# Optimization experiments

Hardware: AMD Instinct MI355X
Metric: run time of the kernel (lower is better)

The kernel has to match this reference:

```python
import jax, jax.numpy as jnp
import numpy as np

N = 1536           # candidates (== pre_nms_k, so pre-selection branch is identity)
H = W = 224        # mask resolution
NCLS = 80
SIGMA = 0.5
POST_NMS_K = 768
SCORE_THRESHOLD = 0.5
EPS = 1e-6


def setup_inputs() -> dict:
    key = jax.random.key(0)
    k1, k2, k3, k4, k5 = jax.random.split(key, 5)
    binary_masks = (jax.random.uniform(k1, (N, H, W)) > 0.5).astype(jnp.float32)
    seg_preds = jax.random.uniform(k2, (N, H, W), dtype=jnp.float32)
    scores = jax.random.uniform(k3, (N,), dtype=jnp.float32)
    cls_labels = jax.random.randint(k4, (N,), 0, NCLS, dtype=jnp.int32)
    cls_factors = jax.random.normal(k5, (N,), dtype=jnp.float32)
    mask_sum = binary_masks.reshape(N, -1).sum(axis=1)  # per-instance area
    return {
        "cls_labels": cls_labels,
        "scores": scores,
        "cls_factors": cls_factors,
        "seg_preds": seg_preds,
        "binary_masks": binary_masks,
        "mask_sum": mask_sum,
    }


def reference(cls_labels, scores, cls_factors, seg_preds, binary_masks, mask_sum):
    """Matrix NMS (SOLOv2) over binary masks; faithful to the torch source.

    Returns fixed-shape, zero-padded (seg_preds, scores, cls_labels, cls_factors)
    with POST_NMS_K rows; padding rows have score 0 / label -1.
    """
    n = scores.shape[0]  # == pre_nms_k, so the torch top-k pre-filter is a no-op
    flat = binary_masks.reshape(n, -1)                    # [N, H*W]
    intersection = flat @ flat.T                          # [N, N] pairwise overlap
    # NOTE: faithful to source: mask_sum.view(1,-1) + mask_sum.view(1,-1)
    # (i.e. 2 * area_j broadcast over rows), reproducing the original's math.
    mask_sum_tile = mask_sum[None, :] + mask_sum[None, :]
    union = mask_sum_tile - intersection
    iou = intersection / (union + EPS)
    iou = jnp.triu(iou, 1)
    labels_match = jnp.triu(
        (cls_labels[None, :] == cls_labels[:, None]).astype(iou.dtype), 1)
    decay_iou = iou * labels_match                        # [N, N]
    compensate_iou = decay_iou.max(axis=0)                # [N]
    comp_mat = compensate_iou[:, None]                    # expand(N,N).T of source
    # gaussian mode
    decay_coefficient = jnp.exp(-(decay_iou ** 2 - comp_mat ** 2) / SIGMA).min(axis=0)
    decayed_scores = scores * decay_coefficient
    valid = decayed_scores >= SCORE_THRESHOLD
    # torch code keeps ORIGINAL scores of surviving rows, then takes top post_nms_k
    sort_key = jnp.where(valid, scores, -1.0)
    _, idx = jax.lax.top_k(sort_key, POST_NMS_K)
    kept_valid = valid[idx]
    out_scores = jnp.where(kept_valid, scores[idx], 0.0)
    out_seg = jnp.where(kept_valid[:, None, None], seg_preds[idx], 0.0)
    out_labels = jnp.where(kept_valid, cls_labels[idx], -1)
    out_factors = jnp.where(kept_valid, cls_factors[idx], 0.0)
    return out_seg, out_scores, out_labels, out_factors
```

## Files before the change

kernel.cpp:

```cpp
#include <hip/hip_runtime.h>
#include <stdint.h>

typedef unsigned long long u64;
typedef unsigned int u32;
typedef unsigned short u16;

#define N_MASKS 1536
#define HW 50176
#define WORDS 784
#define NCLS 80
#define POST_NMS_K 768
#define SEG_ELEMS ((size_t)POST_NMS_K * HW)
#define KEYPAD 2048
#define BITS_BYTES ((size_t)N_MASKS * WORDS * 8)

#define MMAX 96
#define MAXPAIRS (MMAX*(MMAX-1)/2)
#define TW 112
#define TWP 113
#define NTILES (WORDS/TW)

__global__ __launch_bounds__(256) void pack_kernel(const float4* __restrict__ masks,
                                                   u64* __restrict__ bits) {
    int gid = blockIdx.x * blockDim.x + threadIdx.x;
    int wave = gid >> 6;
    int lane = gid & 63;
    float4 v = masks[(size_t)wave * 64 + lane];
    u64 b0 = __ballot(v.x > 0.5f);
    u64 b1 = __ballot(v.y > 0.5f);
    u64 b2 = __ballot(v.z > 0.5f);
    u64 b3 = __ballot(v.w > 0.5f);
    if (lane < 4) {
        u64 w = (lane == 0) ? b0 : (lane == 1) ? b1 : (lane == 2) ? b2 : b3;
        bits[(size_t)wave * 4 + lane] = w;
    }
}

__global__ __launch_bounds__(256) void classnms_kernel(
        const int* __restrict__ labels, const float* __restrict__ scores,
        const float* __restrict__ msum, const u64* __restrict__ bits,
        float* __restrict__ keys) {
    const int cls = blockIdx.x;
    const int tid = threadIdx.x;
    __shared__ int mem[MMAX];
    __shared__ float Sm[MMAX], Sc[MMAX];
    __shared__ u32 compS[MMAX], Ms[MMAX];
    __shared__ u16 lutAB[MAXPAIRS];
    __shared__ u32 Ipair[MAXPAIRS];
    __shared__ u64 rows[MMAX * TWP];
    __shared__ int scan[256];
    __shared__ int mtot;

    const int PER = N_MASKS / 256;
    int lab[PER]; int cnt = 0;
#pragma unroll
    for (int k = 0; k < PER; ++k) { lab[k] = labels[tid * PER + k]; cnt += (lab[k] == cls); }
    scan[tid] = cnt;
    __syncthreads();
    for (int off = 1; off < 256; off <<= 1) {
        int v = scan[tid];
        int u = (tid >= off) ? scan[tid - off] : 0;
        __syncthreads();
        scan[tid] = v + u;
        __syncthreads();
    }
    {
        int o = scan[tid] - cnt;
#pragma unroll
        for (int k = 0; k < PER; ++k)
            if (lab[k] == cls) mem[o++] = tid * PER + k;
    }
    if (tid == 255) mtot = scan[255];
    __syncthreads();
    const int m = mtot;
    const int np = m * (m - 1) / 2;

    for (int b = tid; b < m; b += 256) {
        int g = mem[b];
        Sm[b] = msum[g]; Sc[b] = scores[g];
        compS[b] = 0u; Ms[b] = 0u;
    }
    for (int p = tid; p < np; p += 256) {
        int bb = (int)((1.0 + sqrt(1.0 + 8.0 * (double)p)) * 0.5);
        while (bb * (bb - 1) / 2 > p) --bb;
        while ((bb + 1) * bb / 2 <= p) ++bb;
        int aa = p - bb * (bb - 1) / 2;
        lutAB[p] = (u16)((aa << 8) | bb);
        Ipair[p] = 0u;
    }

    for (int t = 0; t < NTILES; ++t) {
        __syncthreads();
        for (int idx = tid; idx < m * TW; idx += 256) {
            int r = idx / TW, w = idx - r * TW;
            rows[r * TWP + w] = bits[(size_t)mem[r] * WORDS + t * TW + w];
        }
        __syncthreads();
        for (int p = tid; p < np; p += 256) {
            int ab = lutAB[p];
            const u64* ra = &rows[(ab >> 8) * TWP];
            const u64* rb = &rows[(ab & 255) * TWP];
            u32 s = 0;
#pragma unroll 8
            for (int w = 0; w < TW; ++w) s += (u32)__popcll(ra[w] & rb[w]);
            Ipair[p] += s;
        }
    }
    __syncthreads();

    for (int p = tid; p < np; p += 256) {
        int ab = lutAB[p]; int bcol = ab & 255;
        float fI = (float)Ipair[p];
        float D = fI / (2.0f * Sm[bcol] - fI + 1e-6f);
        Ipair[p] = __float_as_uint(D);
        atomicMax(&compS[bcol], __float_as_uint(D));
    }
    __syncthreads();
    for (int p = tid; p < np; p += 256) {
        int ab = lutAB[p]; int aa = ab >> 8; int bcol = ab & 255;
        float D = __uint_as_float(Ipair[p]);
        float ca = __uint_as_float(compS[aa]);
        float v = fmaxf(D * D - ca * ca, 0.0f);
        atomicMax(&Ms[bcol], __float_as_uint(v));
    }
    __syncthreads();
    for (int b = tid; b < m; b += 256) {
        float sc = Sc[b];
        float key = (sc * __expf(-2.0f * __uint_as_float(Ms[b])) >= 0.5f) ? sc : -1.0f;
        keys[mem[b]] = key;
    }
}

__global__ __launch_bounds__(1024) void sortk_kernel(
        const float* __restrict__ keys, const float* __restrict__ scores,
        const int* __restrict__ labels, const float* __restrict__ factors,
        int* __restrict__ sel, float* __restrict__ out_small) {
    __shared__ u64 k2[KEYPAD];
    const int tid = threadIdx.x;
    for (int i = tid; i < KEYPAD; i += 1024) {
        u64 v = 0;
        if (i < N_MASKS) {
            u32 fb = __float_as_uint(keys[i]);
            u32 od = (fb & 0x80000000u) ? ~fb : (fb | 0x80000000u);
            v = ((u64)od << 32) | (u32)(~(u32)i);
        }
        k2[i] = v;
    }
    __syncthreads();
    for (int k = 2; k <= KEYPAD; k <<= 1) {
        for (int j = k >> 1; j > 0; j >>= 1) {
            for (int i = tid; i < KEYPAD; i += 1024) {
                int p = i ^ j;
                if (p > i) {
                    bool desc = ((i & k) == 0);
                    u64 x = k2[i], y = k2[p];
                    if ((x < y) == desc) { k2[i] = y; k2[p] = x; }
                }
            }
            __syncthreads();
        }
    }
    for (int r = tid; r < POST_NMS_K; r += 1024) {
        u64 v = k2[r];
        u32 od = (u32)(v >> 32);
        bool kept = (od >= 0x80000000u);
        int idx = (int)(~(u32)v);
        if (kept) {
            sel[r] = idx;
            out_small[r] = scores[idx];
            out_small[POST_NMS_K + r] = (float)labels[idx];
            out_small[2 * POST_NMS_K + r] = factors[idx];
        } else {
            sel[r] = -1;
            out_small[r] = 0.0f;
            out_small[POST_NMS_K + r] = -1.0f;
            out_small[2 * POST_NMS_K + r] = 0.0f;
        }
    }
}

__global__ __launch_bounds__(256) void gather_kernel(const float4* __restrict__ seg,
                                                     const int* __restrict__ sel,
                                                     float4* __restrict__ out) {
    int row = blockIdx.y;
    int col = blockIdx.x * blockDim.x + threadIdx.x;
    int s = sel[row];
    float4 v = make_float4(0.f, 0.f, 0.f, 0.f);
    if (s >= 0) v = seg[(size_t)s * (HW / 4) + col];
    out[(size_t)row * (HW / 4) + col] = v;
}

extern "C" void kernel_launch(void* const* d_in, const int* in_sizes, int n_in,
                              void* d_out, int out_size, void* d_ws, size_t ws_size,
                              hipStream_t stream) {
    const int* labels = (const int*)d_in[0];
    const float* scores = (const float*)d_in[1];
    const float* factors = (const float*)d_in[2];
    const float* seg = (const float*)d_in[3];
    const float* masks = (const float*)d_in[4];
    const float* msum = (const float*)d_in[5];

    float* out = (float*)d_out;
    u64* bits = (u64*)d_out;

    float* keys = (float*)d_ws;
    int* sel = (int*)(keys + N_MASKS);

    {
        int groups = N_MASKS * (HW / 256);
        pack_kernel<<<groups / 4, 256, 0, stream>>>((const float4*)masks, bits);
    }
    classnms_kernel<<<NCLS, 256, 0, stream>>>(labels, scores, msum, bits, keys);
    sortk_kernel<<<1, 1024, 0, stream>>>(keys, scores, labels, factors, sel,
                                         out + SEG_ELEMS);
    {
        dim3 grid(49, POST_NMS_K);
        gather_kernel<<<grid, 256, 0, stream>>>((const float4*)seg, sel,
                                                (float4*)out);
    }
}
```

Before: 202.2 us.

## Batch loads in pack, gather and classnms tiles; widen classnms blocks

The pack kernel now has each wave handle four float4 groups, producing 16 packed words per wave, and is launched with a quarter of the blocks. The classnms kernel runs 512 threads per block and loads row tiles as 128-bit vectors with four loads in flight before the shared-memory stores. The gather kernel copies four float4 per thread with a bounds check, cutting its grid from 49 to 13 blocks per row. The aim is more memory-level parallelism and less launch and indexing overhead in these bandwidth-bound stages, at the cost of more registers and fewer waves in flight.

```diff
diff --git a/kernel.cpp b/kernel.cpp
--- a/kernel.cpp
+++ b/kernel.cpp
@@ -12,31 +12,39 @@
 #define POST_NMS_K 768
 #define SEG_ELEMS ((size_t)POST_NMS_K * HW)
 #define KEYPAD 2048
-#define BITS_BYTES ((size_t)N_MASKS * WORDS * 8)
 
 #define MMAX 96
 #define MAXPAIRS (MMAX*(MMAX-1)/2)
 #define TW 112
 #define TWP 113
 #define NTILES (WORDS/TW)
+#define CT 512
 
 __global__ __launch_bounds__(256) void pack_kernel(const float4* __restrict__ masks,
                                                    u64* __restrict__ bits) {
     int gid = blockIdx.x * blockDim.x + threadIdx.x;
     int wave = gid >> 6;
     int lane = gid & 63;
-    float4 v = masks[(size_t)wave * 64 + lane];
-    u64 b0 = __ballot(v.x > 0.5f);
-    u64 b1 = __ballot(v.y > 0.5f);
-    u64 b2 = __ballot(v.z > 0.5f);
-    u64 b3 = __ballot(v.w > 0.5f);
+    float4 v[4];
+#pragma unroll
+    for (int g = 0; g < 4; ++g)
+        v[g] = masks[(size_t)wave * 256 + g * 64 + lane];
+    u64 w[16];
+#pragma unroll
+    for (int g = 0; g < 4; ++g) {
+        w[g * 4 + 0] = __ballot(v[g].x > 0.5f);
+        w[g * 4 + 1] = __ballot(v[g].y > 0.5f);
+        w[g * 4 + 2] = __ballot(v[g].z > 0.5f);
+        w[g * 4 + 3] = __ballot(v[g].w > 0.5f);
+    }
     if (lane < 4) {
-        u64 w = (lane == 0) ? b0 : (lane == 1) ? b1 : (lane == 2) ? b2 : b3;
-        bits[(size_t)wave * 4 + lane] = w;
-    }
-}
-
-__global__ __launch_bounds__(256) void classnms_kernel(
+#pragma unroll
+        for (int g = 0; g < 4; ++g)
+            bits[(size_t)wave * 16 + g * 4 + lane] = w[g * 4 + lane];
+    }
+}
+
+__global__ __launch_bounds__(CT) void classnms_kernel(
         const int* __restrict__ labels, const float* __restrict__ scores,
         const float* __restrict__ msum, const u64* __restrict__ bits,
         float* __restrict__ keys) {
@@ -48,20 +56,20 @@
     __shared__ u16 lutAB[MAXPAIRS];
     __shared__ u32 Ipair[MAXPAIRS];
     __shared__ u64 rows[MMAX * TWP];
-    __shared__ int scan[256];
+    __shared__ int scan[CT];
     __shared__ int mtot;
 
-    const int PER = N_MASKS / 256;
+    const int PER = N_MASKS / CT;
     int lab[PER]; int cnt = 0;
 #pragma unroll
     for (int k = 0; k < PER; ++k) { lab[k] = labels[tid * PER + k]; cnt += (lab[k] == cls); }
     scan[tid] = cnt;
     __syncthreads();
-    for (int off = 1; off < 256; off <<= 1) {
-        int v = scan[tid];
-        int u = (tid >= off) ? scan[tid - off] : 0;
-        __syncthreads();
-        scan[tid] = v + u;
+    for (int off = 1; off < CT; off <<= 1) {
+        int vv = scan[tid];
+        int uu = (tid >= off) ? scan[tid - off] : 0;
+        __syncthreads();
+        scan[tid] = vv + uu;
         __syncthreads();
     }
     {
@@ -70,17 +78,17 @@
         for (int k = 0; k < PER; ++k)
             if (lab[k] == cls) mem[o++] = tid * PER + k;
     }
-    if (tid == 255) mtot = scan[255];
+    if (tid == CT - 1) mtot = scan[CT - 1];
     __syncthreads();
     const int m = mtot;
     const int np = m * (m - 1) / 2;
 
-    for (int b = tid; b < m; b += 256) {
+    for (int b = tid; b < m; b += CT) {
         int g = mem[b];
         Sm[b] = msum[g]; Sc[b] = scores[g];
         compS[b] = 0u; Ms[b] = 0u;
     }
-    for (int p = tid; p < np; p += 256) {
+    for (int p = tid; p < np; p += CT) {
         int bb = (int)((1.0 + sqrt(1.0 + 8.0 * (double)p)) * 0.5);
         while (bb * (bb - 1) / 2 > p) --bb;
         while ((bb + 1) * bb / 2 <= p) ++bb;
@@ -89,14 +97,28 @@
         Ipair[p] = 0u;
     }
 
+    const int nb = m * (TW / 2);
     for (int t = 0; t < NTILES; ++t) {
         __syncthreads();
-        for (int idx = tid; idx < m * TW; idx += 256) {
-            int r = idx / TW, w = idx - r * TW;
-            rows[r * TWP + w] = bits[(size_t)mem[r] * WORDS + t * TW + w];
-        }
-        __syncthreads();
-        for (int p = tid; p < np; p += 256) {
+        for (int base = 0; base < nb; base += 4 * CT) {
+            ulonglong2 vv[4]; int dst[4]; bool ok[4];
+#pragma unroll
+            for (int u = 0; u < 4; ++u) {
+                int blk = base + u * CT + tid;
+                ok[u] = (blk < nb);
+                if (ok[u]) {
+                    int r = blk / (TW / 2), k = blk - r * (TW / 2);
+                    dst[u] = r * TWP + 2 * k;
+                    vv[u] = *(const ulonglong2*)(bits + (size_t)mem[r] * WORDS
+                                                 + t * TW + 2 * k);
+                }
+            }
+#pragma unroll
+            for (int u = 0; u < 4; ++u)
+                if (ok[u]) { rows[dst[u]] = vv[u].x; rows[dst[u] + 1] = vv[u].y; }
+        }
+        __syncthreads();
+        for (int p = tid; p < np; p += CT) {
             int ab = lutAB[p];
             const u64* ra = &rows[(ab >> 8) * TWP];
             const u64* rb = &rows[(ab & 255) * TWP];
@@ -108,7 +130,7 @@
     }
     __syncthreads();
 
-    for (int p = tid; p < np; p += 256) {
+    for (int p = tid; p < np; p += CT) {
         int ab = lutAB[p]; int bcol = ab & 255;
         float fI = (float)Ipair[p];
         float D = fI / (2.0f * Sm[bcol] - fI + 1e-6f);
@@ -116,7 +138,7 @@
         atomicMax(&compS[bcol], __float_as_uint(D));
     }
     __syncthreads();
-    for (int p = tid; p < np; p += 256) {
+    for (int p = tid; p < np; p += CT) {
         int ab = lutAB[p]; int aa = ab >> 8; int bcol = ab & 255;
         float D = __uint_as_float(Ipair[p]);
         float ca = __uint_as_float(compS[aa]);
@@ -124,7 +146,7 @@
         atomicMax(&Ms[bcol], __float_as_uint(v));
     }
     __syncthreads();
-    for (int b = tid; b < m; b += 256) {
+    for (int b = tid; b < m; b += CT) {
         float sc = Sc[b];
         float key = (sc * __expf(-2.0f * __uint_as_float(Ms[b])) >= 0.5f) ? sc : -1.0f;
         keys[mem[b]] = key;
@@ -182,12 +204,17 @@
 __global__ __launch_bounds__(256) void gather_kernel(const float4* __restrict__ seg,
                                                      const int* __restrict__ sel,
                                                      float4* __restrict__ out) {
-    int row = blockIdx.y;
-    int col = blockIdx.x * blockDim.x + threadIdx.x;
-    int s = sel[row];
-    float4 v = make_float4(0.f, 0.f, 0.f, 0.f);
-    if (s >= 0) v = seg[(size_t)s * (HW / 4) + col];
-    out[(size_t)row * (HW / 4) + col] = v;
+    const int row = blockIdx.y;
+    const int s = sel[row];
+    const size_t ob = (size_t)row * (HW / 4);
+    const size_t ib = (s >= 0) ? (size_t)s * (HW / 4) : 0;
+    const float4 z = make_float4(0.f, 0.f, 0.f, 0.f);
+#pragma unroll
+    for (int u = 0; u < 4; ++u) {
+        int col = blockIdx.x * 1024 + u * 256 + threadIdx.x;
+        if (col < HW / 4)
+            out[ob + col] = (s >= 0) ? seg[ib + col] : z;
+    }
 }
 
 extern "C" void kernel_launch(void* const* d_in, const int* in_sizes, int n_in,
@@ -207,14 +234,14 @@
     int* sel = (int*)(keys + N_MASKS);
 
     {
-        int groups = N_MASKS * (HW / 256);
-        pack_kernel<<<groups / 4, 256, 0, stream>>>((const float4*)masks, bits);
-    }
-    classnms_kernel<<<NCLS, 256, 0, stream>>>(labels, scores, msum, bits, keys);
+        int waves = N_MASKS * (HW / 1024);
+        pack_kernel<<<waves / 4, 256, 0, stream>>>((const float4*)masks, bits);
+    }
+    classnms_kernel<<<NCLS, CT, 0, stream>>>(labels, scores, msum, bits, keys);
     sortk_kernel<<<1, 1024, 0, stream>>>(keys, scores, labels, factors, sel,
                                          out + SEG_ELEMS);
     {
-        dim3 grid(49, POST_NMS_K);
+        dim3 grid(13, POST_NMS_K);
         gather_kernel<<<grid, 256, 0, stream>>>((const float4*)seg, sel,
                                                 (float4*)out);
     }
```

After: 199.6 us. About the same (-1.3%).
